# Optimization experiments

Measured on AMD Instinct MI355X. Metric: run time of the kernel, lower is better.

The kernel has to match this reference:

```python
import jax, jax.numpy as jnp
import numpy as np

IMG_H, IMG_W = 900, 1600
NUM_CLASSES = 10
NUM_CAMS = 6

# pcdet boxes_to_corners_3d corner template (unit box, centered)
CORNER_TEMPLATE = jnp.array(
    [[1, 1, -1], [1, -1, -1], [-1, -1, -1], [-1, 1, -1],
     [1, 1, 1], [1, -1, 1], [-1, -1, 1], [-1, 1, 1]], dtype=jnp.float32) * 0.5


def boxes_to_corners_3d(boxes):
    # boxes: [N,7] = (x,y,z,dx,dy,dz,heading) -> [N,8,3]
    dims = boxes[:, 3:6]
    corners = dims[:, None, :] * CORNER_TEMPLATE  # [N,8,3]
    yaw = boxes[:, 6]
    c, s = jnp.cos(yaw), jnp.sin(yaw)
    z = jnp.zeros_like(c)
    o = jnp.ones_like(c)
    # rotate_points_along_z: points @ [[c,s,0],[-s,c,0],[0,0,1]]
    rot = jnp.stack([c, s, z, -s, c, z, z, z, o], axis=-1).reshape(-1, 3, 3)
    corners = jnp.einsum('nkj,njm->nkm', corners, rot)
    return corners + boxes[:, None, 0:3]


def box_iou(a, b):
    # a: [M,4], b: [K,4] xyxy -> [M,K]
    lt = jnp.maximum(a[:, None, :2], b[None, :, :2])
    rb = jnp.minimum(a[:, None, 2:], b[None, :, 2:])
    wh = jnp.clip(rb - lt, 0.0)
    inter = wh[..., 0] * wh[..., 1]
    area_a = (a[:, 2] - a[:, 0]) * (a[:, 3] - a[:, 1])
    area_b = (b[:, 2] - b[:, 0]) * (b[:, 3] - b[:, 1])
    union = area_a[:, None] + area_b[None, :] - inter
    return jnp.where(union > 0, inter / union, 0.0)


def _project_boxes(pred_boxes, img_aug_matrix, lidar_aug_matrix, lidar2image):
    # batch index 0 (B=1); returns proj [6,N,4] and valid [6,N]
    N = pred_boxes.shape[0]
    corners = boxes_to_corners_3d(pred_boxes).reshape(-1, 3)  # [N*8,3]
    la = lidar_aug_matrix[0]
    pts = corners - la[:3, 3]
    pts = jnp.linalg.inv(la[:3, :3]) @ pts.T  # [3, N*8]
    l2i = lidar2image[0]
    cc = l2i[:, :3, :3] @ pts + l2i[:, :3, 3][:, :, None]  # [6,3,N*8]
    zc = jnp.clip(cc[:, 2, :], 1e-5, 1e5)
    xy = cc[:, :2, :] / zc[:, None, :]
    cc = jnp.concatenate([xy, zc[:, None, :]], axis=1)
    ia = img_aug_matrix[0]
    cc = ia[:, :3, :3] @ cc + ia[:, :3, 3][:, :, None]
    pix = jnp.transpose(cc[:, :2, :], (0, 2, 1))  # [6, N*8, 2]
    # .long() truncation (non-differentiable in original)
    pix = jax.lax.stop_gradient(pix).astype(jnp.int32)
    px = jnp.clip(pix[..., 0], 0, IMG_W)
    py = jnp.clip(pix[..., 1], 0, IMG_H)
    pix = jnp.stack([px, py], -1).reshape(NUM_CAMS, N, 8, 2).astype(pred_boxes.dtype)
    xy1 = pix.min(axis=2)  # [6,N,2]
    xy2 = pix.max(axis=2)
    valid = jnp.all((xy2 - xy1) > 0, axis=-1)  # [6,N]
    proj = jnp.concatenate([xy1, xy2], axis=-1)  # [6,N,4]
    return proj, valid


def setup_inputs() -> dict:
    rng = np.random.default_rng(0)
    N, M = 4096, 6144
    xy = rng.uniform(-40, 40, (N, 2))
    zc = rng.uniform(-1, 1, (N, 1))
    dims = rng.uniform(1.0, 4.0, (N, 3))
    yaw = rng.uniform(0, 2 * np.pi, (N, 1))
    pred_boxes = np.concatenate([xy, zc, dims, yaw], axis=1).astype(np.float32)
    # 6 cameras: pinhole intrinsics + yaw-spaced extrinsics
    K = np.array([[1000., 0., 800.], [0., 1000., 450.], [0., 0., 1.]])
    l2i = np.zeros((1, NUM_CAMS, 4, 4), np.float32)
    for ci, ang in enumerate(np.linspace(0, 2 * np.pi, NUM_CAMS, endpoint=False)):
        fwd = np.array([np.cos(ang), np.sin(ang), 0.])
        right = np.array([np.sin(ang), -np.cos(ang), 0.])
        down = np.array([0., 0., -1.])
        R = np.stack([right, down, fwd], 0)
        l2i[0, ci, :3, :3] = K @ R
        l2i[0, ci, 3, 3] = 1.0
    img_aug_matrix = np.tile(np.eye(4, dtype=np.float32), (1, NUM_CAMS, 1, 1))
    lidar_aug_matrix = np.eye(4, dtype=np.float32)[None]
    cx = rng.uniform(0, IMG_W, M)
    cy = rng.uniform(0, IMG_H, M)
    w = rng.uniform(20, 300, M)
    h = rng.uniform(20, 300, M)
    det_boxes = np.stack([np.clip(cx - w / 2, 0, IMG_W), np.clip(cy - h / 2, 0, IMG_H),
                          np.clip(cx + w / 2, 0, IMG_W), np.clip(cy + h / 2, 0, IMG_H)], 1).astype(np.float32)
    det_labels = rng.integers(1, NUM_CLASSES + 1, M).astype(np.int32)
    det_scores = rng.uniform(0.05, 1.0, M).astype(np.float32)
    det_batch_idx = np.zeros(M, np.int32)
    det_cam_idx = (np.arange(M) % NUM_CAMS).astype(np.int32)
    return {
        'pred_boxes': jnp.asarray(pred_boxes),
        'img_aug_matrix': jnp.asarray(img_aug_matrix),
        'lidar_aug_matrix': jnp.asarray(lidar_aug_matrix),
        'lidar2image': jnp.asarray(l2i),
        'det_boxes': jnp.asarray(det_boxes),
        'det_labels': jnp.asarray(det_labels),
        'det_scores': jnp.asarray(det_scores),
        'det_batch_idx': jnp.asarray(det_batch_idx),
        'det_cam_idx': jnp.asarray(det_cam_idx),
    }


def reference(pred_boxes, img_aug_matrix, lidar_aug_matrix, lidar2image,
              det_boxes, det_labels, det_scores, det_batch_idx, det_cam_idx):
    proj, valid = _project_boxes(pred_boxes, img_aug_matrix, lidar_aug_matrix, lidar2image)
    label_matrix = jax.nn.one_hot(det_labels - 1, NUM_CLASSES, dtype=det_scores.dtype) * det_scores[:, None]
    probs_sum = jnp.zeros((pred_boxes.shape[0], NUM_CLASSES), dtype=det_scores.dtype)
    for c in range(NUM_CAMS):
        mask = ((det_cam_idx == c) & (det_batch_idx == 0)).astype(det_boxes.dtype)
        iou = box_iou(det_boxes, proj[c]) * mask[:, None]  # [M,N]
        probs_sum = probs_sum + (iou.T @ label_matrix) * valid[c][:, None]  # [N,10]
    denom = 1e-5 + valid.astype(probs_sum.dtype).sum(axis=0)
    box_probs_mean = probs_sum / denom[:, None]
    pred_scores = jnp.nan_to_num(jnp.max(box_probs_mean, axis=-1), nan=0.0)
    pred_labels = jnp.argmax(box_probs_mean, axis=-1) + 1
    return pred_labels, pred_scores
```

## Files before the change

### kernel.cpp

```cpp
#include <hip/hip_runtime.h>
#include <cstdint>
#include <climits>

#pragma clang fp contract(off)

#define NCAM 6
#define NCLS 10
#define NKEY 60
#define IMGW 1600
#define IMGH 900
#define CAP 1024
#define STAGE 512

__device__ __forceinline__ int sat_f2i(float f) {
    if (f != f) return 0;
    if (f >= 2147483648.0f) return INT_MAX;
    if (f <= -2147483648.0f) return INT_MIN;
    return (int)f;
}

__global__ __launch_bounds__(256) void prep_kernel(
        const float*  __restrict__ boxes,
        const float*  __restrict__ ia,
        const float*  __restrict__ la,
        const float*  __restrict__ l2i,
        const float4* __restrict__ det_boxes,
        const int*    __restrict__ det_labels,
        const float*  __restrict__ det_scores,
        const int*    __restrict__ det_batch,
        const int*    __restrict__ det_cam,
        float* __restrict__ projW,
        float* __restrict__ slab,
        int*   __restrict__ cnt,
        int N, int M, int PB) {
    int tid = threadIdx.x;

    if ((int)blockIdx.x < PB) {
        int n = blockIdx.x * 256 + tid;
        if (n >= N) return;
        float bx = boxes[n*7+0], by = boxes[n*7+1], bz = boxes[n*7+2];
        float dx = boxes[n*7+3], dy = boxes[n*7+4], dz = boxes[n*7+5];
        float yaw = boxes[n*7+6];
        float c = (float)cos((double)yaw);
        float s = (float)sin((double)yaw);

        float a00=la[0],a01=la[1],a02=la[2],t0=la[3];
        float a10=la[4],a11=la[5],a12=la[6],t1=la[7];
        float a20=la[8],a21=la[9],a22=la[10],t2=la[11];
        float det = a00*(a11*a22-a12*a21) - a01*(a10*a22-a12*a20) + a02*(a10*a21-a11*a20);
        float id = 1.0f/det;
        float r00=(a11*a22-a12*a21)*id, r01=(a02*a21-a01*a22)*id, r02=(a01*a12-a02*a11)*id;
        float r10=(a12*a20-a10*a22)*id, r11=(a00*a22-a02*a20)*id, r12=(a02*a10-a00*a12)*id;
        float r20=(a10*a21-a11*a20)*id, r21=(a01*a20-a00*a21)*id, r22=(a00*a11-a01*a10)*id;

        float PX[8], PY[8], PZ[8];
        #pragma unroll
        for (int k = 0; k < 8; k++) {
            float sx = ((k==0||k==1||k==4||k==5) ?  0.5f : -0.5f) * dx;
            float sy = ((k==0||k==3||k==4||k==7) ?  0.5f : -0.5f) * dy;
            float sz = ((k>=4)                   ?  0.5f : -0.5f) * dz;
            float cx = sx*c - sy*s + bx;
            float cy = sx*s + sy*c + by;
            float cz = sz + bz;
            float ux = cx - t0, uy = cy - t1, uz = cz - t2;
            PX[k] = r00*ux + r01*uy + r02*uz;
            PY[k] = r10*ux + r11*uy + r12*uz;
            PZ[k] = r20*ux + r21*uy + r22*uz;
        }
        for (int cam = 0; cam < NCAM; cam++) {
            const float* L = l2i + cam*16;
            const float* A = ia  + cam*16;
            int minx = INT_MAX, miny = INT_MAX, maxx = INT_MIN, maxy = INT_MIN;
            #pragma unroll
            for (int k = 0; k < 8; k++) {
                float u = L[0]*PX[k] + L[1]*PY[k] + L[2]*PZ[k]  + L[3];
                float v = L[4]*PX[k] + L[5]*PY[k] + L[6]*PZ[k]  + L[7];
                float w = L[8]*PX[k] + L[9]*PY[k] + L[10]*PZ[k] + L[11];
                float zc = fminf(fmaxf(w, 1e-5f), 100000.0f);
                float x = u / zc, y = v / zc;
                float xx = A[0]*x + A[1]*y + A[2]*zc + A[3];
                float yy = A[4]*x + A[5]*y + A[6]*zc + A[7];
                int pxi = sat_f2i(xx); pxi = min(max(pxi, 0), IMGW);
                int pyi = sat_f2i(yy); pyi = min(max(pyi, 0), IMGH);
                minx = min(minx, pxi); maxx = max(maxx, pxi);
                miny = min(miny, pyi); maxy = max(maxy, pyi);
            }
            float x1 = (float)minx, y1 = (float)miny, x2 = (float)maxx, y2 = (float)maxy;
            float validf = ((x2 - x1) > 0.0f && (y2 - y1) > 0.0f) ? 1.0f : 0.0f;
            projW[(cam*6+0)*N + n] = x1;
            projW[(cam*6+1)*N + n] = y1;
            projW[(cam*6+2)*N + n] = x2;
            projW[(cam*6+3)*N + n] = y2;
            projW[(cam*6+4)*N + n] = (x2 - x1) * (y2 - y1);
            projW[(cam*6+5)*N + n] = validf;
        }
        return;
    }

    int k = (int)blockIdx.x - PB;
    int cam = k / NCLS, cls = k % NCLS;
    __shared__ int wcnt[4];
    __shared__ int running;
    if (tid == 0) running = 0;
    int lane = tid & 63, w = tid >> 6;
    __syncthreads();

    for (int c = 0; c < M; c += 256) {
        int m = c + tid;
        bool pred = false;
        if (m < M) {
            int dc = det_cam[m], db = det_batch[m], dl = det_labels[m] - 1;
            pred = (db == 0) && (dc == cam) && (dl == cls);
        }
        unsigned long long ball = __ballot(pred);
        if (lane == 0) wcnt[w] = __popcll(ball);
        __syncthreads();
        int base = running;
        int pre = 0;
        #pragma unroll
        for (int j = 0; j < 4; j++) pre += (j < w) ? wcnt[j] : 0;
        int tot = wcnt[0] + wcnt[1] + wcnt[2] + wcnt[3];
        if (pred) {
            int pos = base + pre + __popcll(ball & ((1ull << lane) - 1ull));
            float4 b = det_boxes[m];
            float area = (b.z - b.x) * (b.w - b.y);
            float4* o = (float4*)(slab + ((size_t)k * CAP + pos) * 8);
            o[0] = b;
            o[1] = make_float4(area, det_scores[m], 0.0f, 0.0f);
        }
        __syncthreads();
        if (tid == 0) running += tot;
    }
    __syncthreads();
    if (tid == 0) cnt[k] = running;
}

__global__ __launch_bounds__(256) void main_kernel(
        const float* __restrict__ projW,
        const float* __restrict__ slab,
        const int*   __restrict__ cnt,
        float*       __restrict__ partial,
        int N) {
    int tid = threadIdx.x;
    int k = blockIdx.y;
    int cam = k / NCLS;
    int box = blockIdx.x * 256 + tid;
    __shared__ float4 sd[STAGE * 2];

    int nk = cnt[k];
    float Px1 = 0, Py1 = 0, Px2 = 0, Py2 = 0, Pa = 0, Pv = 0;
    if (box < N) {
        Px1 = projW[(cam*6+0)*N + box];
        Py1 = projW[(cam*6+1)*N + box];
        Px2 = projW[(cam*6+2)*N + box];
        Py2 = projW[(cam*6+3)*N + box];
        Pa  = projW[(cam*6+4)*N + box];
        Pv  = projW[(cam*6+5)*N + box];
    }
    float acc = 0.0f;
    const float4* gsl = (const float4*)slab;

    for (int base = 0; base < nk; base += STAGE) {
        int cc = min(STAGE, nk - base);
        __syncthreads();
        for (int i = tid; i < cc * 2; i += 256)
            sd[i] = gsl[((size_t)k * CAP + base) * 2 + i];
        __syncthreads();
        if (box < N) {
            for (int m = 0; m < cc; m++) {
                float4 b = sd[2*m];
                float4 q = sd[2*m+1];
                float ltx = fmaxf(b.x, Px1);
                float lty = fmaxf(b.y, Py1);
                float rbx = fminf(b.z, Px2);
                float rby = fminf(b.w, Py2);
                float iw = fmaxf(rbx - ltx, 0.0f);
                float ih = fmaxf(rby - lty, 0.0f);
                float inter = iw * ih;
                float uni = (q.x + Pa) - inter;
                float r = __fdividef(inter, uni);
                float iou = (uni > 0.0f) ? r : 0.0f;
                acc += iou * q.y;
            }
        }
    }
    if (box < N) partial[(size_t)k * N + box] = acc * Pv;
}

__global__ __launch_bounds__(256) void reduce_kernel(
        const float* __restrict__ partial,
        const float* __restrict__ projW,
        float* __restrict__ out, int N) {
    int n = blockIdx.x * 256 + threadIdx.x;
    if (n >= N) return;
    float p[NCLS];
    #pragma unroll
    for (int c = 0; c < NCLS; c++) p[c] = 0.0f;
    #pragma unroll
    for (int cam = 0; cam < NCAM; cam++)
        #pragma unroll
        for (int c = 0; c < NCLS; c++)
            p[c] += partial[(size_t)(cam * NCLS + c) * N + n];
    float nv = 0.0f;
    #pragma unroll
    for (int cam = 0; cam < NCAM; cam++) nv += projW[(cam*6+5)*N + n];
    float denom = 1e-5f + nv;
    float best = -1e30f; int bk = 0;
    #pragma unroll
    for (int c = 0; c < NCLS; c++) {
        float v = p[c] / denom;
        if (v > best) { best = v; bk = c; }
    }
    out[n]     = (float)(bk + 1);
    out[N + n] = best;
}

extern "C" void kernel_launch(void* const* d_in, const int* in_sizes, int n_in,
                              void* d_out, int out_size, void* d_ws, size_t ws_size,
                              hipStream_t stream) {
    const float*  pred_boxes = (const float*)d_in[0];
    const float*  ia         = (const float*)d_in[1];
    const float*  la         = (const float*)d_in[2];
    const float*  l2i        = (const float*)d_in[3];
    const float4* det_boxes  = (const float4*)d_in[4];
    const int*    det_labels = (const int*)d_in[5];
    const float*  det_scores = (const float*)d_in[6];
    const int*    det_batch  = (const int*)d_in[7];
    const int*    det_cam    = (const int*)d_in[8];
    float* out = (float*)d_out;

    int N = in_sizes[0] / 7;
    int M = in_sizes[4] / 4;
    int PB = (N + 255) / 256;

    char* w = (char*)d_ws;
    float* slab    = (float*)w;
    size_t off = (size_t)NKEY * CAP * 8 * 4;
    float* projW   = (float*)(w + off);
    off += (size_t)36 * N * 4;
    float* partial = (float*)(w + off);
    off += (size_t)NKEY * N * 4;
    int*   cnt     = (int*)(w + off);

    prep_kernel<<<PB + NKEY, 256, 0, stream>>>(pred_boxes, ia, la, l2i,
                                               det_boxes, det_labels, det_scores,
                                               det_batch, det_cam,
                                               projW, slab, cnt, N, M, PB);
    main_kernel<<<dim3(PB, NKEY), 256, 0, stream>>>(projW, slab, cnt, partial, N);
    reduce_kernel<<<PB, 256, 0, stream>>>(partial, projW, out, N);
}
```

Before: 118.6 us.

## Compact detections per wave without block syncs and read slab directly in IoU loop

Result: slower. 122.1 us (+3.0%).

```diff
diff --git a/kernel.cpp b/kernel.cpp
--- a/kernel.cpp
+++ b/kernel.cpp
@@ -9,8 +9,6 @@
 #define NKEY 60
 #define IMGW 1600
 #define IMGH 900
-#define CAP 1024
-#define STAGE 512
 
 __device__ __forceinline__ int sat_f2i(float f) {
     if (f != f) return 0;
@@ -32,7 +30,7 @@
         float* __restrict__ projW,
         float* __restrict__ slab,
         int*   __restrict__ cnt,
-        int N, int M, int PB) {
+        int N, int M, int PB, int CAPW) {
     int tid = threadIdx.x;
 
     if ((int)blockIdx.x < PB) {
@@ -99,40 +97,30 @@
 
     int k = (int)blockIdx.x - PB;
     int cam = k / NCLS, cls = k % NCLS;
-    __shared__ int wcnt[4];
-    __shared__ int running;
-    if (tid == 0) running = 0;
-    int lane = tid & 63, w = tid >> 6;
-    __syncthreads();
-
-    for (int c = 0; c < M; c += 256) {
-        int m = c + tid;
+    int w = tid >> 6, lane = tid & 63;
+    int per = (M + 3) >> 2;
+    int m0 = w * per, m1 = min(m0 + per, M);
+    float* base = slab + (size_t)(k * 4 + w) * CAPW * 8;
+    int pos = 0;
+    for (int c = m0; c < m1; c += 64) {
+        int m = c + lane;
         bool pred = false;
-        if (m < M) {
+        if (m < m1) {
             int dc = det_cam[m], db = det_batch[m], dl = det_labels[m] - 1;
             pred = (db == 0) && (dc == cam) && (dl == cls);
         }
         unsigned long long ball = __ballot(pred);
-        if (lane == 0) wcnt[w] = __popcll(ball);
-        __syncthreads();
-        int base = running;
-        int pre = 0;
-        #pragma unroll
-        for (int j = 0; j < 4; j++) pre += (j < w) ? wcnt[j] : 0;
-        int tot = wcnt[0] + wcnt[1] + wcnt[2] + wcnt[3];
         if (pred) {
-            int pos = base + pre + __popcll(ball & ((1ull << lane) - 1ull));
+            int p = pos + __popcll(ball & ((1ull << lane) - 1ull));
             float4 b = det_boxes[m];
             float area = (b.z - b.x) * (b.w - b.y);
-            float4* o = (float4*)(slab + ((size_t)k * CAP + pos) * 8);
+            float4* o = (float4*)(base + (size_t)p * 8);
             o[0] = b;
             o[1] = make_float4(area, det_scores[m], 0.0f, 0.0f);
         }
-        __syncthreads();
-        if (tid == 0) running += tot;
-    }
-    __syncthreads();
-    if (tid == 0) cnt[k] = running;
+        pos += __popcll(ball);
+    }
+    if (lane == 0) cnt[k * 4 + w] = pos;
 }
 
 __global__ __launch_bounds__(256) void main_kernel(
@@ -140,48 +128,39 @@
         const float* __restrict__ slab,
         const int*   __restrict__ cnt,
         float*       __restrict__ partial,
-        int N) {
+        int N, int CAPW) {
     int tid = threadIdx.x;
     int k = blockIdx.y;
     int cam = k / NCLS;
     int box = blockIdx.x * 256 + tid;
-    __shared__ float4 sd[STAGE * 2];
-
-    int nk = cnt[k];
-    float Px1 = 0, Py1 = 0, Px2 = 0, Py2 = 0, Pa = 0, Pv = 0;
-    if (box < N) {
-        Px1 = projW[(cam*6+0)*N + box];
-        Py1 = projW[(cam*6+1)*N + box];
-        Px2 = projW[(cam*6+2)*N + box];
-        Py2 = projW[(cam*6+3)*N + box];
-        Pa  = projW[(cam*6+4)*N + box];
-        Pv  = projW[(cam*6+5)*N + box];
-    }
+    int bidx = min(box, N - 1);
+
+    float Px1 = projW[(cam*6+0)*N + bidx];
+    float Py1 = projW[(cam*6+1)*N + bidx];
+    float Px2 = projW[(cam*6+2)*N + bidx];
+    float Py2 = projW[(cam*6+3)*N + bidx];
+    float Pa  = projW[(cam*6+4)*N + bidx];
+    float Pv  = projW[(cam*6+5)*N + bidx];
+
     float acc = 0.0f;
-    const float4* gsl = (const float4*)slab;
-
-    for (int base = 0; base < nk; base += STAGE) {
-        int cc = min(STAGE, nk - base);
-        __syncthreads();
-        for (int i = tid; i < cc * 2; i += 256)
-            sd[i] = gsl[((size_t)k * CAP + base) * 2 + i];
-        __syncthreads();
-        if (box < N) {
-            for (int m = 0; m < cc; m++) {
-                float4 b = sd[2*m];
-                float4 q = sd[2*m+1];
-                float ltx = fmaxf(b.x, Px1);
-                float lty = fmaxf(b.y, Py1);
-                float rbx = fminf(b.z, Px2);
-                float rby = fminf(b.w, Py2);
-                float iw = fmaxf(rbx - ltx, 0.0f);
-                float ih = fmaxf(rby - lty, 0.0f);
-                float inter = iw * ih;
-                float uni = (q.x + Pa) - inter;
-                float r = __fdividef(inter, uni);
-                float iou = (uni > 0.0f) ? r : 0.0f;
-                acc += iou * q.y;
-            }
+    #pragma unroll
+    for (int sub = 0; sub < 4; sub++) {
+        int nk = cnt[k * 4 + sub];
+        const float4* bp = (const float4*)(slab + (size_t)(k * 4 + sub) * CAPW * 8);
+        for (int m = 0; m < nk; m++) {
+            float4 b = bp[2*m];
+            float4 q = bp[2*m+1];
+            float ltx = fmaxf(b.x, Px1);
+            float lty = fmaxf(b.y, Py1);
+            float rbx = fminf(b.z, Px2);
+            float rby = fminf(b.w, Py2);
+            float iw = fmaxf(rbx - ltx, 0.0f);
+            float ih = fmaxf(rby - lty, 0.0f);
+            float inter = iw * ih;
+            float uni = (q.x + Pa) - inter;
+            float r = __fdividef(inter, uni);
+            float iou = (uni > 0.0f) ? r : 0.0f;
+            acc += iou * q.y;
         }
     }
     if (box < N) partial[(size_t)k * N + box] = acc * Pv;
@@ -232,10 +211,11 @@
     int N = in_sizes[0] / 7;
     int M = in_sizes[4] / 4;
     int PB = (N + 255) / 256;
+    int CAPW = (M + 3) / 4;
 
     char* w = (char*)d_ws;
     float* slab    = (float*)w;
-    size_t off = (size_t)NKEY * CAP * 8 * 4;
+    size_t off = (size_t)NKEY * 4 * CAPW * 8 * 4;
     float* projW   = (float*)(w + off);
     off += (size_t)36 * N * 4;
     float* partial = (float*)(w + off);
@@ -245,7 +225,7 @@
     prep_kernel<<<PB + NKEY, 256, 0, stream>>>(pred_boxes, ia, la, l2i,
                                                det_boxes, det_labels, det_scores,
                                                det_batch, det_cam,
-                                               projW, slab, cnt, N, M, PB);
-    main_kernel<<<dim3(PB, NKEY), 256, 0, stream>>>(projW, slab, cnt, partial, N);
+                                               projW, slab, cnt, N, M, PB, CAPW);
+    main_kernel<<<dim3(PB, NKEY), 256, 0, stream>>>(projW, slab, cnt, partial, N, CAPW);
     reduce_kernel<<<PB, 256, 0, stream>>>(partial, projW, out, N);
 }
```
